# Kernel optimization log

Hardware: AMD Instinct MI355X
Metric: run time of the kernel (lower is better)

The kernel has to match this reference:

```python
import jax, jax.numpy as jnp
import numpy as np

N_NODES = 50000
N_EDGES = 800000
IN_FEATS = 128
N_HIDDEN = 64
OUT_FEATS = 40
DIM = 8  # pseudo-coordinate dimension
K = 1    # n_kernels


def setup_inputs() -> dict:
    key = jax.random.key(0)
    ks = jax.random.split(key, 12)
    inp = {
        "features": jax.random.normal(ks[0], (N_NODES, IN_FEATS), dtype=jnp.float32),
        "edge_weight": jax.random.normal(ks[1], (N_EDGES, DIM), dtype=jnp.float32),
        "src": jax.random.randint(ks[2], (N_EDGES,), 0, N_NODES),
        "dst": jax.random.randint(ks[3], (N_EDGES,), 0, N_NODES),
        # layer 1 params (fc has no bias in DGL GMMConv; separate additive bias)
        "W1": jax.random.normal(ks[4], (IN_FEATS, K * N_HIDDEN), dtype=jnp.float32) * (1.0 / np.sqrt(IN_FEATS)),
        "b1": jnp.zeros((N_HIDDEN,), dtype=jnp.float32),
        "mu1": jax.random.normal(ks[5], (K, DIM), dtype=jnp.float32) * 0.1,
        "inv_sigma1": jnp.ones((K, DIM), dtype=jnp.float32),
        # layer 2 params
        "W2": jax.random.normal(ks[6], (N_HIDDEN, K * OUT_FEATS), dtype=jnp.float32) * (1.0 / np.sqrt(N_HIDDEN)),
        "b2": jnp.zeros((OUT_FEATS,), dtype=jnp.float32),
        "mu2": jax.random.normal(ks[7], (K, DIM), dtype=jnp.float32) * 0.1,
        "inv_sigma2": jnp.ones((K, DIM), dtype=jnp.float32),
    }
    return inp


def gmm_conv(x, pseudo, src, dst, W, b, mu, inv_sigma, out_feats):
    # x: [N, in], pseudo: [E, DIM], W: [in, K*out]
    h = (x @ W).reshape(-1, K, out_feats)                      # [N, K, out]
    # gaussian mixture weights per edge/kernel: [E, K]
    diff = pseudo[:, None, :] - mu[None, :, :]                 # [E, K, DIM]
    gw = jnp.exp(-0.5 * jnp.sum(diff * diff * (inv_sigma[None] ** 2), axis=-1))
    # gather src feats, weight, sum over kernels: [E, out]
    msg = jnp.einsum("ekf,ek->ef", h[src], gw)
    agg = jax.ops.segment_sum(msg, dst, num_segments=N_NODES)  # [N, out]
    return agg + b


def reference(features, edge_weight, src, dst, W1, b1, mu1, inv_sigma1, W2, b2, mu2, inv_sigma2):
    x = gmm_conv(features, edge_weight, src, dst, W1, b1, mu1, inv_sigma1, N_HIDDEN)
    x = gmm_conv(x, edge_weight, src, dst, W2, b2, mu2, inv_sigma2, OUT_FEATS)
    return jax.nn.log_softmax(x, axis=1)
```

## Files before the change

### kernel.cpp

```cpp
#include <hip/hip_runtime.h>
#include <hip/hip_fp16.h>
#include <math.h>

#define N_NODES 50000
#define N_EDGES 800000
#define IN_FEATS 128
#define N_HIDDEN 64
#define OUT_FEATS 40
#define DIM 8
#define SCAN_NB ((N_NODES + 255) / 256)
#define GT_TILES ((N_NODES + 63) / 64)
#define FILL_NB 1024

typedef _Float16 half8 __attribute__((ext_vector_type(8)));
typedef float floatx4 __attribute__((ext_vector_type(4)));

__device__ __forceinline__ int wave_incl_scan(int x, int lane) {
#pragma unroll
    for (int off = 1; off < 64; off <<= 1) {
        int v = __shfl_up(x, off, 64);
        if (lane >= off) x += v;
    }
    return x;
}

__global__ __launch_bounds__(256) void edge_kernel(
    const int* __restrict__ src, const int* __restrict__ dst,
    const float* __restrict__ ew,
    const float* __restrict__ mu1, const float* __restrict__ is1,
    const float* __restrict__ mu2, const float* __restrict__ is2,
    int* __restrict__ counts, int2* __restrict__ tmp)
{
    int e = blockIdx.x * 256 + threadIdx.x;
    if (e >= N_EDGES) return;
    atomicAdd(&counts[dst[e]], 1);
    float s1 = 0.f, s2 = 0.f;
#pragma unroll
    for (int d = 0; d < DIM; ++d) {
        float v = ew[e * DIM + d];
        float d1 = v - mu1[d]; float a1 = is1[d];
        float d2 = v - mu2[d]; float a2 = is2[d];
        s1 += d1 * d1 * a1 * a1;
        s2 += d2 * d2 * a2 * a2;
    }
    __half2 g = __floats2half2_rn(expf(-0.5f * s1), expf(-0.5f * s2));
    int2 rec;
    rec.x = src[e];
    rec.y = *reinterpret_cast<int*>(&g);
    tmp[e] = rec;
}

__global__ __launch_bounds__(256) void scan_kernel(const int* __restrict__ counts,
                                                   int* __restrict__ offsets,
                                                   int* __restrict__ cursor,
                                                   int* __restrict__ partials) {
    const int tid = threadIdx.x, bid = blockIdx.x;
    int i = bid * 256 + tid;
    int lane = tid & 63, wid = tid >> 6;
    int x = (i < N_NODES) ? counts[i] : 0;
    int incl = wave_incl_scan(x, lane);
    __shared__ int wsum[4];
    __shared__ int sExc, sTot;
    if (lane == 63) wsum[wid] = incl;
    __syncthreads();
    int base = 0;
#pragma unroll
    for (int w = 0; w < 4; ++w)
        if (w < wid) base += wsum[w];
    int lexcl = base + incl - x;
    if (tid == 255) sTot = base + incl;
    __syncthreads();
    if (tid == 0) {
        int T = sTot;
        if (bid == 0) {
            __hip_atomic_store(&partials[0], (T << 2) | 2,
                               __ATOMIC_RELAXED, __HIP_MEMORY_SCOPE_AGENT);
            sExc = 0;
        } else {
            __hip_atomic_store(&partials[bid], (T << 2) | 1,
                               __ATOMIC_RELAXED, __HIP_MEMORY_SCOPE_AGENT);
            int sum = 0, pb = bid - 1;
            while (true) {
                int v = __hip_atomic_load(&partials[pb],
                                          __ATOMIC_RELAXED, __HIP_MEMORY_SCOPE_AGENT);
                if (v == 0) continue;
                sum += v >> 2;
                if ((v & 3) == 2) break;
                --pb;
            }
            __hip_atomic_store(&partials[bid], ((sum + T) << 2) | 2,
                               __ATOMIC_RELAXED, __HIP_MEMORY_SCOPE_AGENT);
            sExc = sum;
        }
    }
    __syncthreads();
    int E = sExc;
    if (i < N_NODES) {
        int v = E + lexcl;
        offsets[i] = v;
        cursor[i]  = v;
    }
    if (bid == SCAN_NB - 1 && tid == 0) offsets[N_NODES] = N_EDGES;
}

__global__ __launch_bounds__(256) void fillgemm_kernel(
    const float* __restrict__ features, const float* __restrict__ W1,
    const int* __restrict__ dst, const int2* __restrict__ tmp,
    int* __restrict__ cursor, int2* __restrict__ csr,
    __half* __restrict__ h1)
{
    const int tid = threadIdx.x;
    __shared__ __align__(16) __half WT[64][136];

    if (blockIdx.x >= GT_TILES) {
        int fb = blockIdx.x - GT_TILES;
        for (int e = fb * 256 + tid; e < N_EDGES; e += FILL_NB * 256) {
            int pos = atomicAdd(&cursor[dst[e]], 1);
            csr[pos] = tmp[e];
        }
        return;
    }

    int nodeBase = blockIdx.x * 64;
    for (int rep = 0; rep < 32; ++rep) {
        int idx = tid + rep * 256;
        int k = idx >> 6, n = idx & 63;
        WT[n][k] = __float2half(W1[idx]);
    }
    __syncthreads();

    int lane = tid & 63, w = tid >> 6;
    int m = lane & 15, quad = lane >> 4;
    int row = nodeBase + w * 16 + m;
    int rowc = (row < N_NODES) ? row : (N_NODES - 1);
    const float* fr = features + (size_t)rowc * IN_FEATS;

    floatx4 acc0 = {0.f,0.f,0.f,0.f}, acc1 = acc0, acc2 = acc0, acc3 = acc0;
#pragma unroll
    for (int kc = 0; kc < 4; ++kc) {
        float4 fa = *(const float4*)(fr + kc * 32 + quad * 8);
        float4 fb = *(const float4*)(fr + kc * 32 + quad * 8 + 4);
        union { half8 v; __half2 h2[4]; } A;
        A.h2[0] = __floats2half2_rn(fa.x, fa.y);
        A.h2[1] = __floats2half2_rn(fa.z, fa.w);
        A.h2[2] = __floats2half2_rn(fb.x, fb.y);
        A.h2[3] = __floats2half2_rn(fb.z, fb.w);
        half8 b0 = *(const half8*)&WT[ 0 + m][kc * 32 + quad * 8];
        half8 b1 = *(const half8*)&WT[16 + m][kc * 32 + quad * 8];
        half8 b2 = *(const half8*)&WT[32 + m][kc * 32 + quad * 8];
        half8 b3 = *(const half8*)&WT[48 + m][kc * 32 + quad * 8];
        acc0 = __builtin_amdgcn_mfma_f32_16x16x32_f16(A.v, b0, acc0, 0, 0, 0);
        acc1 = __builtin_amdgcn_mfma_f32_16x16x32_f16(A.v, b1, acc1, 0, 0, 0);
        acc2 = __builtin_amdgcn_mfma_f32_16x16x32_f16(A.v, b2, acc2, 0, 0, 0);
        acc3 = __builtin_amdgcn_mfma_f32_16x16x32_f16(A.v, b3, acc3, 0, 0, 0);
    }
    int nodeRow = nodeBase + w * 16 + quad * 4;
#pragma unroll
    for (int r = 0; r < 4; ++r) {
        int n = nodeRow + r;
        if (n < N_NODES) {
            size_t base = (size_t)n * N_HIDDEN + m;
            h1[base +  0] = __float2half(acc0[r]);
            h1[base + 16] = __float2half(acc1[r]);
            h1[base + 32] = __float2half(acc2[r]);
            h1[base + 48] = __float2half(acc3[r]);
        }
    }
}

__global__ __launch_bounds__(256) void agg1_gemm2_kernel(const __half* __restrict__ h,
                                                         const int* __restrict__ offsets,
                                                         const int2* __restrict__ csr,
                                                         const float* __restrict__ b,
                                                         const float* __restrict__ W2,
                                                         __half* __restrict__ h2) {
    __shared__ float xs[8][64];
    const unsigned* h32 = (const unsigned*)h;
    const int tid = threadIdx.x;
    const int w = tid >> 6, lane = tid & 63;
    const int hf = lane >> 5, p = lane & 31;
    const int ln = w * 2 + hf;
    const int n = blockIdx.x * 8 + ln;
    int beg = offsets[n], end = offsets[n + 1];

    float ax = 0.f, ay = 0.f;
    int j = beg;
    for (; j + 4 <= end; j += 4) {
        int2 r0 = csr[j + 0], r1 = csr[j + 1], r2 = csr[j + 2], r3 = csr[j + 3];
        unsigned v0 = h32[(size_t)r0.x * 32 + p];
        unsigned v1 = h32[(size_t)r1.x * 32 + p];
        unsigned v2 = h32[(size_t)r2.x * 32 + p];
        unsigned v3 = h32[(size_t)r3.x * 32 + p];
        float g0 = __low2float(*reinterpret_cast<__half2*>(&r0.y));
        float g1 = __low2float(*reinterpret_cast<__half2*>(&r1.y));
        float g2 = __low2float(*reinterpret_cast<__half2*>(&r2.y));
        float g3 = __low2float(*reinterpret_cast<__half2*>(&r3.y));
        float2 f0 = __half22float2(*reinterpret_cast<__half2*>(&v0));
        float2 f1 = __half22float2(*reinterpret_cast<__half2*>(&v1));
        float2 f2 = __half22float2(*reinterpret_cast<__half2*>(&v2));
        float2 f3 = __half22float2(*reinterpret_cast<__half2*>(&v3));
        ax += f0.x * g0; ay += f0.y * g0;
        ax += f1.x * g1; ay += f1.y * g1;
        ax += f2.x * g2; ay += f2.y * g2;
        ax += f3.x * g3; ay += f3.y * g3;
    }
    for (; j < end; ++j) {
        int2 r = csr[j];
        unsigned v = h32[(size_t)r.x * 32 + p];
        float g = __low2float(*reinterpret_cast<__half2*>(&r.y));
        float2 f = __half22float2(*reinterpret_cast<__half2*>(&v));
        ax += f.x * g; ay += f.y * g;
    }
    float2 bb = *(const float2*)&b[2 * p];
    *(float2*)&xs[ln][2 * p] = make_float2(ax + bb.x, ay + bb.y);
    __syncthreads();

    for (int o = tid; o < 8 * OUT_FEATS; o += 256) {
        int node = o / OUT_FEATS, t = o % OUT_FEATS;
        const float* xr = xs[node];
        float acc = 0.f;
#pragma unroll
        for (int k = 0; k < N_HIDDEN; ++k)
            acc += xr[k] * W2[k * OUT_FEATS + t];
        h2[(size_t)(blockIdx.x * 8 + node) * OUT_FEATS + t] = __float2half(acc);
    }
}

__global__ __launch_bounds__(256) void agg2_kernel(const __half* __restrict__ h,
                                                   const int* __restrict__ offsets,
                                                   const int2* __restrict__ csr,
                                                   const float* __restrict__ b,
                                                   float* __restrict__ out) {
    const unsigned* h32 = (const unsigned*)h;
    const int tid = threadIdx.x;
    const int w = tid >> 6, lane = tid & 63;
    const int hf = lane >> 5, p = lane & 31;
    const int n = blockIdx.x * 8 + w * 2 + hf;
    const int pc = (p < 20) ? p : 19;
    int beg = offsets[n], end = offsets[n + 1];

    float ax = 0.f, ay = 0.f;
    int j = beg;
    for (; j + 4 <= end; j += 4) {
        int2 r0 = csr[j + 0], r1 = csr[j + 1], r2 = csr[j + 2], r3 = csr[j + 3];
        unsigned v0 = h32[(size_t)r0.x * 20 + pc];
        unsigned v1 = h32[(size_t)r1.x * 20 + pc];
        unsigned v2 = h32[(size_t)r2.x * 20 + pc];
        unsigned v3 = h32[(size_t)r3.x * 20 + pc];
        float g0 = __high2float(*reinterpret_cast<__half2*>(&r0.y));
        float g1 = __high2float(*reinterpret_cast<__half2*>(&r1.y));
        float g2 = __high2float(*reinterpret_cast<__half2*>(&r2.y));
        float g3 = __high2float(*reinterpret_cast<__half2*>(&r3.y));
        float2 f0 = __half22float2(*reinterpret_cast<__half2*>(&v0));
        float2 f1 = __half22float2(*reinterpret_cast<__half2*>(&v1));
        float2 f2 = __half22float2(*reinterpret_cast<__half2*>(&v2));
        float2 f3 = __half22float2(*reinterpret_cast<__half2*>(&v3));
        ax += f0.x * g0; ay += f0.y * g0;
        ax += f1.x * g1; ay += f1.y * g1;
        ax += f2.x * g2; ay += f2.y * g2;
        ax += f3.x * g3; ay += f3.y * g3;
    }
    for (; j < end; ++j) {
        int2 r = csr[j];
        unsigned v = h32[(size_t)r.x * 20 + pc];
        float g = __high2float(*reinterpret_cast<__half2*>(&r.y));
        float2 f = __half22float2(*reinterpret_cast<__half2*>(&v));
        ax += f.x * g; ay += f.y * g;
    }

    bool valid = (p < 20);
    float vx = valid ? ax + b[2 * p]     : -INFINITY;
    float vy = valid ? ay + b[2 * p + 1] : -INFINITY;
    float m = fmaxf(vx, vy);
#pragma unroll
    for (int off = 16; off; off >>= 1)
        m = fmaxf(m, __shfl_xor(m, off, 32));
    float ex = valid ? (expf(vx - m) + expf(vy - m)) : 0.f;
#pragma unroll
    for (int off = 16; off; off >>= 1)
        ex += __shfl_xor(ex, off, 32);
    float ls = logf(ex);
    if (valid) {
        float2 o = make_float2(vx - m - ls, vy - m - ls);
        *(float2*)&out[(size_t)n * OUT_FEATS + 2 * p] = o;
    }
}

extern "C" void kernel_launch(void* const* d_in, const int* in_sizes, int n_in,
                              void* d_out, int out_size, void* d_ws, size_t ws_size,
                              hipStream_t stream) {
    const float* features    = (const float*)d_in[0];
    const float* edge_weight = (const float*)d_in[1];
    const int*   src         = (const int*)d_in[2];
    const int*   dst         = (const int*)d_in[3];
    const float* W1          = (const float*)d_in[4];
    const float* b1          = (const float*)d_in[5];
    const float* mu1         = (const float*)d_in[6];
    const float* is1         = (const float*)d_in[7];
    const float* W2          = (const float*)d_in[8];
    const float* b2          = (const float*)d_in[9];
    const float* mu2         = (const float*)d_in[10];
    const float* is2         = (const float*)d_in[11];
    float* out = (float*)d_out;

    int2*   csr     = (int2*)d_ws;
    int2*   tmp     = csr + N_EDGES;
    __half* h1      = (__half*)(tmp + N_EDGES);
    __half* h2      = h1 + (size_t)N_NODES * N_HIDDEN;
    int*    counts  = (int*)(h2 + (size_t)N_NODES * OUT_FEATS);
    int*    partials= counts + N_NODES;
    int*    cursor  = partials + 256;
    int*    offsets = cursor + N_NODES;

    hipMemsetAsync(counts, 0, (N_NODES + 256) * sizeof(int), stream);

    edge_kernel<<<(N_EDGES + 255) / 256, 256, 0, stream>>>(
        src, dst, edge_weight, mu1, is1, mu2, is2, counts, tmp);

    scan_kernel<<<SCAN_NB, 256, 0, stream>>>(counts, offsets, cursor, partials);

    fillgemm_kernel<<<GT_TILES + FILL_NB, 256, 0, stream>>>(
        features, W1, dst, tmp, cursor, csr, h1);

    agg1_gemm2_kernel<<<N_NODES / 8, 256, 0, stream>>>(h1, offsets, csr, b1, W2, h2);

    agg2_kernel<<<N_NODES / 8, 256, 0, stream>>>(h2, offsets, csr, b2, out);
}
```

Before: 268.9 us.

## Move Gaussian weight computation into CSR fill and slim histogram kernel

Replaces the per-edge kernel, which computed counts, the Gaussian weights and a temporary record array, with a histogram-only kernel that reads dst as int4 and issues four atomics per thread. The Gaussian weight and src packing now happen inside the fill blocks of fillgemm, which write directly into the CSR. This removes the write and re-read of the 6.4MB temporary array. In exchange, the edge_weight and src reads move into the scattered fill loop, where they overlap with the GEMM blocks.

```diff
diff --git a/kernel.cpp b/kernel.cpp
--- a/kernel.cpp
+++ b/kernel.cpp
@@ -24,30 +24,15 @@
     return x;
 }
 
-__global__ __launch_bounds__(256) void edge_kernel(
-    const int* __restrict__ src, const int* __restrict__ dst,
-    const float* __restrict__ ew,
-    const float* __restrict__ mu1, const float* __restrict__ is1,
-    const float* __restrict__ mu2, const float* __restrict__ is2,
-    int* __restrict__ counts, int2* __restrict__ tmp)
-{
-    int e = blockIdx.x * 256 + threadIdx.x;
-    if (e >= N_EDGES) return;
-    atomicAdd(&counts[dst[e]], 1);
-    float s1 = 0.f, s2 = 0.f;
-#pragma unroll
-    for (int d = 0; d < DIM; ++d) {
-        float v = ew[e * DIM + d];
-        float d1 = v - mu1[d]; float a1 = is1[d];
-        float d2 = v - mu2[d]; float a2 = is2[d];
-        s1 += d1 * d1 * a1 * a1;
-        s2 += d2 * d2 * a2 * a2;
-    }
-    __half2 g = __floats2half2_rn(expf(-0.5f * s1), expf(-0.5f * s2));
-    int2 rec;
-    rec.x = src[e];
-    rec.y = *reinterpret_cast<int*>(&g);
-    tmp[e] = rec;
+__global__ __launch_bounds__(256) void hist_kernel(const int* __restrict__ dst,
+                                                   int* __restrict__ counts) {
+    int i = blockIdx.x * 256 + threadIdx.x;
+    if (i * 4 >= N_EDGES) return;
+    int4 d = ((const int4*)dst)[i];
+    atomicAdd(&counts[d.x], 1);
+    atomicAdd(&counts[d.y], 1);
+    atomicAdd(&counts[d.z], 1);
+    atomicAdd(&counts[d.w], 1);
 }
 
 __global__ __launch_bounds__(256) void scan_kernel(const int* __restrict__ counts,
@@ -105,7 +90,10 @@
 
 __global__ __launch_bounds__(256) void fillgemm_kernel(
     const float* __restrict__ features, const float* __restrict__ W1,
-    const int* __restrict__ dst, const int2* __restrict__ tmp,
+    const int* __restrict__ src, const int* __restrict__ dst,
+    const float* __restrict__ ew,
+    const float* __restrict__ mu1, const float* __restrict__ is1,
+    const float* __restrict__ mu2, const float* __restrict__ is2,
     int* __restrict__ cursor, int2* __restrict__ csr,
     __half* __restrict__ h1)
 {
@@ -115,8 +103,23 @@
     if (blockIdx.x >= GT_TILES) {
         int fb = blockIdx.x - GT_TILES;
         for (int e = fb * 256 + tid; e < N_EDGES; e += FILL_NB * 256) {
+            const float4* ew4 = (const float4*)(ew + (size_t)e * DIM);
+            float4 wa = ew4[0], wb = ew4[1];
+            float v[8] = {wa.x, wa.y, wa.z, wa.w, wb.x, wb.y, wb.z, wb.w};
+            float s1 = 0.f, s2 = 0.f;
+#pragma unroll
+            for (int d = 0; d < DIM; ++d) {
+                float d1 = v[d] - mu1[d]; float a1 = is1[d];
+                float d2 = v[d] - mu2[d]; float a2 = is2[d];
+                s1 += d1 * d1 * a1 * a1;
+                s2 += d2 * d2 * a2 * a2;
+            }
+            __half2 g = __floats2half2_rn(expf(-0.5f * s1), expf(-0.5f * s2));
+            int2 rec;
+            rec.x = src[e];
+            rec.y = *reinterpret_cast<int*>(&g);
             int pos = atomicAdd(&cursor[dst[e]], 1);
-            csr[pos] = tmp[e];
+            csr[pos] = rec;
         }
         return;
     }
@@ -304,8 +307,7 @@
     float* out = (float*)d_out;
 
     int2*   csr     = (int2*)d_ws;
-    int2*   tmp     = csr + N_EDGES;
-    __half* h1      = (__half*)(tmp + N_EDGES);
+    __half* h1      = (__half*)(csr + N_EDGES);
     __half* h2      = h1 + (size_t)N_NODES * N_HIDDEN;
     int*    counts  = (int*)(h2 + (size_t)N_NODES * OUT_FEATS);
     int*    partials= counts + N_NODES;
@@ -314,13 +316,12 @@
 
     hipMemsetAsync(counts, 0, (N_NODES + 256) * sizeof(int), stream);
 
-    edge_kernel<<<(N_EDGES + 255) / 256, 256, 0, stream>>>(
-        src, dst, edge_weight, mu1, is1, mu2, is2, counts, tmp);
+    hist_kernel<<<(N_EDGES / 4 + 255) / 256, 256, 0, stream>>>(dst, counts);
 
     scan_kernel<<<SCAN_NB, 256, 0, stream>>>(counts, offsets, cursor, partials);
 
     fillgemm_kernel<<<GT_TILES + FILL_NB, 256, 0, stream>>>(
-        features, W1, dst, tmp, cursor, csr, h1);
+        features, W1, src, dst, edge_weight, mu1, is1, mu2, is2, cursor, csr, h1);
 
     agg1_gemm2_kernel<<<N_NODES / 8, 256, 0, stream>>>(h1, offsets, csr, b1, W2, h2);
 
```

Result: faster. 261.7 us (-2.7%).
